# Kernel optimization log

Hardware: AMD Instinct MI355X
Metric: run time of the kernel (lower is better)

The kernel has to match this reference:

```python
import jax, jax.numpy as jnp
import numpy as np
from jax.scipy.special import erf

T_OBS = 1.0
T_CONTROL = 3.0
B = 4096
NT = 2048
DT0 = 0.002


def _moments(t_obs):
    t_avg = t_obs / 2.0
    t2_avg = t_obs ** 2 / 3.0
    C_t = t2_avg - t_avg ** 2
    return t_avg, t2_avg, C_t


def _sigma_move(sig_f, sig_a, xi_f, xi_v, t_obs):
    # 3x3 posterior covariance over (a, f, v), per get_Sigma_move_noSM
    xi_f_ = xi_f * (np.sqrt(t_obs) / sig_f)
    xi_v_ = xi_v * (np.sqrt(t_obs) / sig_f)
    t_avg, t2_avg, C_t = _moments(t_obs)
    det_inv = (1 + 1 / xi_f_ ** 2) * (C_t + 1 / xi_v_ ** 2) + t_avg ** 2 / xi_f_ ** 2
    pre = sig_f ** 2 / t_obs / det_inv ** 2
    Sff = (C_t + 1 / xi_v_ ** 2) ** 2 + C_t * t_avg ** 2
    Sfv = t_avg * (1 / (xi_f_ * xi_v_) ** 2 - C_t)
    Svv = (t_avg / xi_f_ ** 2) ** 2 + C_t * (1 + 1 / xi_f_ ** 2) ** 2
    zz = jnp.zeros(())
    row0 = jnp.stack([sig_a ** 2, zz, zz])
    row1 = jnp.stack([zz, pre * Sff, pre * Sfv])
    row2 = jnp.stack([zz, pre * Sfv, pre * Svv])
    return jnp.stack([row0, row1, row2])


def _sigma_stat(sig_f, xi_f, xi_v, t_obs):
    # 2x2 posterior covariance over (f, v), per get_Sigma_stat_noSM
    xi_f_ = xi_f * (np.sqrt(t_obs) / sig_f)
    xi_v_ = xi_v * (np.sqrt(t_obs) / sig_f)
    t_avg, t2_avg, C_t = _moments(t_obs)
    det_inv = (1 + 1 / xi_f_ ** 2) * (C_t + 1 / xi_v_ ** 2) + t_avg ** 2 / xi_f_ ** 2
    pre = sig_f ** 2 / t_obs
    Sff = pre / (1 + 1 / xi_f_ ** 2) ** 2
    Sfv = pre * (t_avg / (xi_f_ ** 2 + 1)) / det_inv
    Svv = pre * ((t_avg / xi_f_ ** 2) ** 2 + C_t * (1 + 1 / xi_f_ ** 2) ** 2) / det_inv ** 2
    return jnp.stack([jnp.stack([Sff, Sfv]), jnp.stack([Sfv, Svv])])


def _threshold(sig_f, xi_f, xi_v, d0, t_obs):
    xi_f_ = xi_f * (np.sqrt(t_obs) / sig_f)
    xi_v_ = xi_v * (np.sqrt(t_obs) / sig_f)
    t_avg, t2_avg, C_t = _moments(t_obs)
    log_arg = 1 + xi_v_ ** 2 * (C_t + t2_avg / (1 + xi_f_ ** 2))
    det_ratio = t_obs / sig_f ** 2 * (C_t + 1 / xi_v_ ** 2 + t2_avg / (1 + xi_f_ ** 2))
    thresh_sq = (jnp.log(log_arg) - 2 * d0) / det_ratio
    return jnp.sqrt(jax.nn.relu(thresh_sq))


def _control_weights(tau, t_wait, alpha, T_control):
    # Control-A gain profiles over the (shared) time grid tau [NT].
    Tm = T_control - jnp.mean(t_wait)
    rem = jax.nn.relu(Tm - tau)
    w_f = alpha * rem / Tm
    w_v = alpha * rem ** 2 / (2 * Tm ** 2)
    w_o_move = jnp.stack([w_f, w_v])          # [2, NT]
    w_o_stat = w_f[None, :]                   # [1, NT]
    w_tx = alpha * jnp.ones_like(tau)         # [NT]
    w_tv = alpha * rem / Tm                   # [NT]
    return w_o_move, w_o_stat, w_tx, w_tv


def _get_L(u_t, x_t, z, dt, Sinv_m, Sinv_s, det_m, det_s, W_m, W_s, q,
           wo_m, wo_s, w_tx, w_tv, g, sig_a):
    z_noa = z[:, 1:]
    num_t = u_t.shape[1]
    g2 = g * g
    resid = u_t - w_tx[None, :] * x_t                          # [B, T]
    data_quad = 0.5 * (dt / g2) * jnp.sum(resid ** 2, axis=-1)  # [B]

    def branch(Sinv, W, zz, wo, with_ctrl_v):
        S_vv = Sinv[-1, -1]
        S_vo = Sinv[-1, :-1]
        S_oo = Sinv[:-1, :-1]
        W_v = W[-1]
        W_o = W[:-1]
        A = S_oo[None] + (dt[:, None, None] / g2) * (wo @ wo.T)[None]  # [B,no,no]
        A_inv = jnp.linalg.inv(A)
        det_A = jnp.linalg.det(A)
        Woz = zz @ W_o.T                                       # [B, no]
        Wvz = zz @ W_v                                         # [B]
        d = (dt[:, None] / g2) * jnp.einsum('it,bt->bi', wo, resid)
        J_r = Woz @ S_oo.T + Wvz[:, None] * S_vo[None, :] + d   # [B, no]
        if with_ctrl_v:
            J_v = S_vo[None, :] + (dt[:, None] / g2) * (wo @ w_tv)[None, :]
            J = (S_vv * Wvz + Woz @ S_vo
                 + (dt / g2) * jnp.einsum('t,bt->b', w_tv, resid)
                 - jnp.einsum('bi,bij,bj->b', J_r, A_inv, J_v))
            k = (S_vv + (dt / g2) * jnp.sum(w_tv ** 2)
                 - jnp.einsum('bi,bij,bj->b', J_v, A_inv, J_v))
        else:
            J_v = jnp.broadcast_to(S_vo[None, :], J_r.shape)
            J = (S_vv * Wvz + Woz @ S_vo
                 - jnp.einsum('bi,bij,bj->b', J_r, A_inv, J_v))
            k = S_vv - jnp.einsum('bi,bij,bj->b', J_v, A_inv, J_v)
        Z = (0.5 * jnp.einsum('bi,ij,jk,kl,bl->b', zz, W, Sinv, W, zz)
             + data_quad
             - 0.5 * jnp.einsum('bi,bij,bj->b', J_r, A_inv, J_r)
             - 0.5 * J * J / k)
        return J, k, Z, det_A

    J_m, k_m, Z_m, detA_m = branch(Sinv_m, W_m, z, wo_m, True)
    J_s, k_s, Z_s, detA_s = branch(Sinv_s, W_s, z_noa, wo_s, False)

    pre_m = k_m * detA_m * det_m * sig_a ** 2
    pre_s = k_s * detA_s * det_s
    erf_m = (1 + 0.5 * erf((J_m - k_m * q) / jnp.sqrt(2 * k_m))
             - 0.5 * erf((J_m + k_m * q) / jnp.sqrt(2 * k_m)))
    erf_s = (0.5 * erf((J_s + k_s * q) / jnp.sqrt(2 * k_s))
             - 0.5 * erf((J_s - k_s * q) / jnp.sqrt(2 * k_s)))
    L_m = jnp.exp(-Z_m) * erf_m / jnp.sqrt(pre_m)
    L_s = jnp.exp(-Z_s) * erf_s / jnp.sqrt(pre_s)
    return jnp.sum(num_t * jnp.log(2 * np.pi * g2 / dt) - jnp.log(L_m + L_s))


def _forward(u_t, x_t, z, t, t_wait, u_t_SM, x_t_SM, z_SM, t_SM, t_wait_SM,
             hsig_f, hsig_w, hxi_f, hxi_w, hxi_v, delta0, halpha, hg, hW_aa, hsig_a):
    sig_f = jnp.exp(hsig_f[0]); sig_w = jnp.exp(hsig_w[0])
    xi_f = jnp.exp(hxi_f[0]); xi_w = jnp.exp(hxi_w[0]); xi_v = jnp.exp(hxi_v[0])
    d0 = delta0[0]; alpha = jnp.exp(halpha[0]); g = jnp.exp(hg[0])
    W_aa = jnp.exp(hW_aa[0]); sig_a = jnp.exp(hsig_a[0])
    one = jnp.ones(())

    dt = t[:, 1] - t[:, 0]
    dt_SM = t_SM[:, 1] - t[:, 0]  # matches original code (uses t[:,0])

    # ---- no self-motion branch ----
    Sig_m = _sigma_move(sig_f, sig_a, xi_f, xi_v, T_OBS)
    Sig_s = _sigma_stat(sig_f, xi_f, xi_v, T_OBS)
    Sinv_m = jnp.linalg.inv(Sig_m); det_m = jnp.linalg.det(Sig_m)
    Sinv_s = jnp.linalg.inv(Sig_s); det_s = jnp.linalg.det(Sig_s)
    W_m = jnp.diag(jnp.stack([W_aa, one, alpha]))
    W_s = jnp.diag(jnp.stack([one, alpha]))
    q = _threshold(sig_f, xi_f, xi_v, d0, T_OBS)
    wo_m, wo_s, w_tx, w_tv = _control_weights(t[0], t_wait, alpha, T_CONTROL)
    L1 = _get_L(u_t, x_t, z, dt, Sinv_m, Sinv_s, det_m, det_s,
                W_m, W_s, q, wo_m, wo_s, w_tx, w_tv, g, sig_a)

    # ---- self-motion branch: noise inflated by sig_w / xi_w, gain scaled by W_aa ----
    sig_eff = jnp.sqrt(sig_f ** 2 + sig_w ** 2)
    xi_v_eff = jnp.sqrt(xi_v ** 2 + xi_w ** 2)
    alpha_sm = alpha * W_aa
    Sig_m2 = _sigma_move(sig_eff, sig_a, xi_f, xi_v_eff, T_OBS)
    Sig_s2 = _sigma_stat(sig_eff, xi_f, xi_v_eff, T_OBS)
    Sinv_m2 = jnp.linalg.inv(Sig_m2); det_m2 = jnp.linalg.det(Sig_m2)
    Sinv_s2 = jnp.linalg.inv(Sig_s2); det_s2 = jnp.linalg.det(Sig_s2)
    W_m2 = jnp.diag(jnp.stack([W_aa, one, alpha_sm]))
    W_s2 = jnp.diag(jnp.stack([one, alpha_sm]))
    q2 = _threshold(sig_eff, xi_f, xi_v_eff, d0, T_OBS)
    wo_m2, wo_s2, w_tx2, w_tv2 = _control_weights(t_SM[0], t_wait_SM, alpha_sm, T_CONTROL)
    L2 = _get_L(u_t_SM, x_t_SM, z_SM, dt_SM, Sinv_m2, Sinv_s2, det_m2, det_s2,
                W_m2, W_s2, q2, wo_m2, wo_s2, w_tx2, w_tv2, g, sig_a)
    return L1 + L2


def setup_inputs() -> dict:
    key = jax.random.key(0)
    ks = jax.random.split(key, 8)
    f32 = jnp.float32
    tau = jnp.arange(NT, dtype=f32) * DT0
    t = jnp.broadcast_to(tau, (B, NT))
    return {
        'u_t': 0.05 * jax.random.normal(ks[0], (B, NT), f32),
        'x_t': 0.05 * jax.random.normal(ks[1], (B, NT), f32),
        'z': 0.1 * jax.random.normal(ks[2], (B, 3), f32),
        't': t,
        't_wait': 0.3 * jax.random.uniform(ks[3], (B,), f32),
        'u_t_SM': 0.05 * jax.random.normal(ks[4], (B, NT), f32),
        'x_t_SM': 0.05 * jax.random.normal(ks[5], (B, NT), f32),
        'z_SM': 0.1 * jax.random.normal(ks[6], (B, 3), f32),
        't_SM': t,
        't_wait_SM': 0.3 * jax.random.uniform(ks[7], (B,), f32),
        'hsig_f': jnp.array([-0.7], f32),
        'hsig_w': jnp.array([-1.0], f32),
        'hxi_f': jnp.array([0.0], f32),
        'hxi_w': jnp.array([-0.5], f32),
        'hxi_v': jnp.array([0.0], f32),
        'delta0': jnp.array([-0.5], f32),
        'halpha': jnp.array([-0.3], f32),
        'hg': jnp.array([0.0], f32),
        'hW_aa': jnp.array([-0.2], f32),
        'hsig_a': jnp.array([-0.7], f32),
    }


def reference(u_t, x_t, z, t, t_wait, u_t_SM, x_t_SM, z_SM, t_SM, t_wait_SM,
              hsig_f, hsig_w, hxi_f, hxi_w, hxi_v, delta0, halpha, hg, hW_aa, hsig_a):
    return _forward(u_t, x_t, z, t, t_wait, u_t_SM, x_t_SM, z_SM, t_SM, t_wait_SM,
                    hsig_f, hsig_w, hxi_f, hxi_w, hxi_v, delta0, halpha, hg, hW_aa, hsig_a)
```

## Files before the change

kernel.cpp:

```cpp
#include <hip/hip_runtime.h>
#include <math.h>

#ifndef M_PI
#define M_PI 3.14159265358979323846
#endif

#define TPB 256


__device__ double block_sum_d(double v, double* buf) {
    int tid = threadIdx.x;
    buf[tid] = v;
    __syncthreads();
    for (int o = TPB / 2; o > 0; o >>= 1) {
        if (tid < o) buf[tid] += buf[tid + o];
        __syncthreads();
    }
    double r = buf[0];
    __syncthreads();
    return r;
}

__global__ __launch_bounds__(TPB) void precompute_kernel(
    const float* __restrict__ t, const float* __restrict__ t_wait,
    const float* __restrict__ t_SM, const float* __restrict__ t_wait_SM,
    const float* __restrict__ hsig_f, const float* __restrict__ hsig_w,
    const float* __restrict__ hxi_f, const float* __restrict__ hxi_w,
    const float* __restrict__ hxi_v, const float* __restrict__ delta0,
    const float* __restrict__ halpha, const float* __restrict__ hg,
    const float* __restrict__ hW_aa, const float* __restrict__ hsig_a,
    int B, int NT, double* __restrict__ ws, float* __restrict__ out)
{
    __shared__ double buf[TPB];
    __shared__ double sh[2];
    int tid = threadIdx.x;

    double s1 = 0.0, s2 = 0.0;
    for (int i = tid; i < B; i += TPB) {
        s1 += (double)t_wait[i];
        s2 += (double)t_wait_SM[i];
    }
    double tw1 = block_sum_d(s1, buf);
    double tw2 = block_sum_d(s2, buf);
    if (tid == 0) { sh[0] = 3.0 - tw1 / (double)B; sh[1] = 3.0 - tw2 / (double)B; }
    __syncthreads();
    double Tm1 = sh[0], Tm2 = sh[1];

    double a2 = 0, a3 = 0, a4 = 0, b2 = 0, b3 = 0, b4 = 0;
    for (int i = tid; i < NT; i += TPB) {
        double r1 = Tm1 - (double)t[i];    r1 = r1 > 0.0 ? r1 : 0.0;
        double r2 = Tm2 - (double)t_SM[i]; r2 = r2 > 0.0 ? r2 : 0.0;
        double r1s = r1 * r1, r2s = r2 * r2;
        a2 += r1s; a3 += r1s * r1; a4 += r1s * r1s;
        b2 += r2s; b3 += r2s * r2; b4 += r2s * r2s;
    }
    a2 = block_sum_d(a2, buf); a3 = block_sum_d(a3, buf); a4 = block_sum_d(a4, buf);
    b2 = block_sum_d(b2, buf); b3 = block_sum_d(b3, buf); b4 = block_sum_d(b4, buf);
    if (tid != 0) return;

    out[0] = 0.0f;

    double sig_f = exp((double)hsig_f[0]);
    double sig_w = exp((double)hsig_w[0]);
    double xi_f  = exp((double)hxi_f[0]);
    double xi_w  = exp((double)hxi_w[0]);
    double xi_v  = exp((double)hxi_v[0]);
    double d0    = (double)delta0[0];
    double alpha = exp((double)halpha[0]);
    double g     = exp((double)hg[0]);
    double W_aa  = exp((double)hW_aa[0]);
    double sig_a = exp((double)hsig_a[0]);
    double g2 = g * g, sig_a2 = sig_a * sig_a;

    for (int L = 0; L < 2; ++L) {
        double sf, xv, ab, Tm, S2, S3, S4;
        if (L == 0) { sf = sig_f; xv = xi_v; ab = alpha; Tm = Tm1; S2 = a2; S3 = a3; S4 = a4; }
        else {
            sf = sqrt(sig_f * sig_f + sig_w * sig_w);
            xv = sqrt(xi_v * xi_v + xi_w * xi_w);
            ab = alpha * W_aa; Tm = Tm2; S2 = b2; S3 = b3; S4 = b4;
        }
        double xf_ = xi_f / sf, xv_ = xv / sf;
        double t_avg = 0.5, t2_avg = 1.0 / 3.0, C_t = 1.0 / 12.0;
        double ixf2 = 1.0 / (xf_ * xf_), ixv2 = 1.0 / (xv_ * xv_);
        double det_inv = (1.0 + ixf2) * (C_t + ixv2) + t_avg * t_avg * ixf2;

        double pre_m = sf * sf / (det_inv * det_inv);
        double Sff = (C_t + ixv2) * (C_t + ixv2) + C_t * t_avg * t_avg;
        double Sfv = t_avg * (ixf2 * ixv2 - C_t);
        double Svv = (t_avg * ixf2) * (t_avg * ixf2) + C_t * (1.0 + ixf2) * (1.0 + ixf2);
        double m11 = pre_m * Sff, m12 = pre_m * Sfv, m22 = pre_m * Svv;
        double detB = m11 * m22 - m12 * m12;
        double Sm00 = 1.0 / sig_a2;
        double Sm11 = m22 / detB, Sm12 = -m12 / detB, Sm22 = m11 / detB;
        double det_m = sig_a2 * detB;

        double pre_s = sf * sf;
        double Sffs = pre_s / ((1.0 + ixf2) * (1.0 + ixf2));
        double Sfvs = pre_s * (t_avg / (xf_ * xf_ + 1.0)) / det_inv;
        double Svvs = pre_s * ((t_avg * ixf2) * (t_avg * ixf2) + C_t * (1.0 + ixf2) * (1.0 + ixf2)) / (det_inv * det_inv);
        double det_s = Sffs * Svvs - Sfvs * Sfvs;
        double Ss00 = Svvs / det_s, Ss01 = -Sfvs / det_s, Ss11 = Sffs / det_s;

        double log_arg = 1.0 + xv_ * xv_ * (C_t + t2_avg / (1.0 + xf_ * xf_));
        double det_ratio = (1.0 / (sf * sf)) * (C_t + 1.0 / (xv_ * xv_) + t2_avg / (1.0 + xf_ * xf_));
        double tq = (log(log_arg) - 2.0 * d0) / det_ratio;
        double q = sqrt(tq > 0.0 ? tq : 0.0);

        double kf = ab / Tm, kv = ab / (2.0 * Tm * Tm);
        double Gff = kf * kf * S2, Gfv = kf * kv * S3, Gvv = kv * kv * S4;

        double* w = ws + L * 32;
        w[0] = Sm00; w[1] = 0.0; w[2] = 0.0; w[3] = Sm11; w[4] = Sm12; w[5] = Sm22;
        w[6] = Ss00; w[7] = Ss01; w[8] = Ss11;
        w[9] = det_m; w[10] = det_s; w[11] = q;
        w[12] = Gff; w[13] = Gfv; w[14] = Gvv;
        w[15] = ab; w[16] = kf; w[17] = kv; w[18] = Tm;
        w[19] = W_aa; w[20] = g2; w[21] = sig_a2;
    }
}

__global__ __launch_bounds__(TPB) void stream_kernel(
    const float* __restrict__ u_t, const float* __restrict__ x_t,
    const float* __restrict__ u_SM, const float* __restrict__ x_SM,
    const float* __restrict__ t, const float* __restrict__ t_SM,
    int NT, int B, const double* __restrict__ ws, float* __restrict__ mom)
{
    int wid  = blockIdx.x * (TPB / 64) + (threadIdx.x >> 6);
    int lane = threadIdx.x & 63;
    int row  = wid >> 1, half = wid & 1;
    int n4 = NT >> 2, h4 = n4 >> 1;

    float ab1 = (float)ws[15],      Tm1 = (float)ws[18];
    float ab2 = (float)ws[32 + 15], Tm2 = (float)ws[32 + 18];

    size_t off = (size_t)row * (size_t)NT;
    const float4* U1 = (const float4*)(u_t + off);
    const float4* X1 = (const float4*)(x_t + off);
    const float4* U2 = (const float4*)(u_SM + off);
    const float4* X2 = (const float4*)(x_SM + off);
    const float4* T1 = (const float4*)t;
    const float4* T2 = (const float4*)t_SM;

    float s2a = 0, r1a = 0, r2a = 0, s2b = 0, r1b = 0, r2b = 0;
    int iend = (half + 1) * h4;
    for (int i = half * h4 + lane; i < iend; i += 64) {
        float4 u = U1[i], x = X1[i], ta = T1[i];
        float4 uu = U2[i], xx = X2[i], tb = T2[i];
        float uc[4]  = {u.x, u.y, u.z, u.w};
        float xc[4]  = {x.x, x.y, x.z, x.w};
        float tc[4]  = {ta.x, ta.y, ta.z, ta.w};
        float uuc[4] = {uu.x, uu.y, uu.z, uu.w};
        float xxc[4] = {xx.x, xx.y, xx.z, xx.w};
        float tbc[4] = {tb.x, tb.y, tb.z, tb.w};
#pragma unroll
        for (int j = 0; j < 4; ++j) {
            float resid = fmaf(-ab1, xc[j], uc[j]);
            float rem = fmaxf(Tm1 - tc[j], 0.0f);
            s2a = fmaf(resid, resid, s2a);
            r1a = fmaf(rem, resid, r1a);
            r2a = fmaf(rem * rem, resid, r2a);
            float rs = fmaf(-ab2, xxc[j], uuc[j]);
            float rm = fmaxf(Tm2 - tbc[j], 0.0f);
            s2b = fmaf(rs, rs, s2b);
            r1b = fmaf(rm, rs, r1b);
            r2b = fmaf(rm * rm, rs, r2b);
        }
    }
#pragma unroll
    for (int o = 32; o >= 1; o >>= 1) {
        s2a += __shfl_xor(s2a, o); r1a += __shfl_xor(r1a, o); r2a += __shfl_xor(r2a, o);
        s2b += __shfl_xor(s2b, o); r1b += __shfl_xor(r1b, o); r2b += __shfl_xor(r2b, o);
    }
    if (lane == 0) {
        int W = 2 * B;
        mom[0 * W + wid] = s2a; mom[1 * W + wid] = r1a; mom[2 * W + wid] = r2a;
        mom[3 * W + wid] = s2b; mom[4 * W + wid] = r1b; mom[5 * W + wid] = r2b;
    }
}

__device__ double epilogue(const double* __restrict__ S, int NT,
                           double s2, double R1, double R2,
                           double z0, double z1, double z2, double dtb)
{
    double Sm00 = S[0], Sm01 = S[1], Sm02 = S[2], Sm11 = S[3], Sm12 = S[4], Sm22 = S[5];
    double Ss00 = S[6], Ss01 = S[7], Ss11 = S[8];
    double det_m = S[9], det_s = S[10], q = S[11];
    double Gff = S[12], Gfv = S[13], Gvv = S[14];
    double ab = S[15], kf = S[16], kv = S[17];
    double W_aa = S[19], g2 = S[20], sig_a2 = S[21];

    double cb = dtb / g2;
    double df = kf * R1, dv = kv * R2;
    double data_quad = 0.5 * cb * s2;

    double Svo0 = Sm02, Svo1 = Sm12, Svv = Sm22;
    double A00 = Sm00 + cb * Gff, A01 = Sm01 + cb * Gfv, A11 = Sm11 + cb * Gvv;
    double detA = A00 * A11 - A01 * A01;
    double i00 = A11 / detA, i01 = -A01 / detA, i11 = A00 / detA;
    double Woz0 = W_aa * z0, Woz1 = z1, Wvz = ab * z2;
    double Jr0 = Woz0 * Sm00 + Woz1 * Sm01 + Wvz * Svo0 + cb * df;
    double Jr1 = Woz0 * Sm01 + Woz1 * Sm11 + Wvz * Svo1 + cb * dv;
    double Jv0 = Svo0 + cb * Gff, Jv1 = Svo1 + cb * Gfv;
    double AiJv0 = i00 * Jv0 + i01 * Jv1, AiJv1 = i01 * Jv0 + i11 * Jv1;
    double AiJr0 = i00 * Jr0 + i01 * Jr1, AiJr1 = i01 * Jr0 + i11 * Jr1;
    double Jm = Svv * Wvz + Woz0 * Svo0 + Woz1 * Svo1 + cb * df
              - (Jr0 * AiJv0 + Jr1 * AiJv1);
    double km = Svv + cb * Gff - (Jv0 * AiJv0 + Jv1 * AiJv1);
    double y0 = W_aa * z0, y1 = z1, y2 = ab * z2;
    double zq = y0 * y0 * Sm00 + y1 * y1 * Sm11 + y2 * y2 * Sm22
              + 2.0 * (y0 * y1 * Sm01 + y0 * y2 * Sm02 + y1 * y2 * Sm12);
    double Zm = 0.5 * zq + data_quad - 0.5 * (Jr0 * AiJr0 + Jr1 * AiJr1) - 0.5 * Jm * Jm / km;

    double As = Ss00 + cb * Gff;
    double Wozs = z1, Wvzs = ab * z2;
    double Jrs = Wozs * Ss00 + Wvzs * Ss01 + cb * df;
    double Jvs = Ss01;
    double Js = Ss11 * Wvzs + Wozs * Ss01 - Jrs * Jvs / As;
    double ks = Ss11 - Jvs * Jvs / As;
    double ys1 = ab * z2;
    double zqs = z1 * z1 * Ss00 + 2.0 * z1 * ys1 * Ss01 + ys1 * ys1 * Ss11;
    double Zs = 0.5 * zqs + data_quad - 0.5 * Jrs * Jrs / As - 0.5 * Js * Js / ks;

    double pre_m = km * detA * det_m * sig_a2;
    double pre_s = ks * As * det_s;
    double sm = sqrt(2.0 * km), ss = sqrt(2.0 * ks);
    double em = 1.0 + 0.5 * erf((Jm - km * q) / sm) - 0.5 * erf((Jm + km * q) / sm);
    double es = 0.5 * erf((Js + ks * q) / ss) - 0.5 * erf((Js - ks * q) / ss);
    double Lm = exp(-Zm) * em / sqrt(pre_m);
    double Ls = exp(-Zs) * es / sqrt(pre_s);
    return (double)NT * log(2.0 * M_PI * g2 / dtb) - log(Lm + Ls);
}

__global__ __launch_bounds__(TPB) void epilogue_kernel(
    const float* __restrict__ z, const float* __restrict__ z_SM,
    const float* __restrict__ t, const float* __restrict__ t_SM,
    int NT, int B, const double* __restrict__ ws,
    const float* __restrict__ mom, float* __restrict__ out)
{
    int row = blockIdx.x * TPB + threadIdx.x;
    double c = 0.0;
    if (row < B) {
        int W = 2 * B;
        double S2a = (double)mom[0 * W + 2 * row] + (double)mom[0 * W + 2 * row + 1];
        double R1a = (double)mom[1 * W + 2 * row] + (double)mom[1 * W + 2 * row + 1];
        double R2a = (double)mom[2 * W + 2 * row] + (double)mom[2 * W + 2 * row + 1];
        double S2b = (double)mom[3 * W + 2 * row] + (double)mom[3 * W + 2 * row + 1];
        double R1b = (double)mom[4 * W + 2 * row] + (double)mom[4 * W + 2 * row + 1];
        double R2b = (double)mom[5 * W + 2 * row] + (double)mom[5 * W + 2 * row + 1];
        size_t off = (size_t)row * (size_t)NT;
        double dtb1 = (double)t[off + 1] - (double)t[off];
        double dtb2 = (double)t_SM[off + 1] - (double)t[off];
        double z0 = (double)z[row * 3 + 0], z1 = (double)z[row * 3 + 1], z2 = (double)z[row * 3 + 2];
        double w0 = (double)z_SM[row * 3 + 0], w1 = (double)z_SM[row * 3 + 1], w2 = (double)z_SM[row * 3 + 2];
        c = epilogue(ws, NT, S2a, R1a, R2a, z0, z1, z2, dtb1)
          + epilogue(ws + 32, NT, S2b, R1b, R2b, w0, w1, w2, dtb2);
    }
    __shared__ double buf[TPB];
    int tid = threadIdx.x;
    buf[tid] = c;
    __syncthreads();
    for (int o = TPB / 2; o > 0; o >>= 1) {
        if (tid < o) buf[tid] += buf[tid + o];
        __syncthreads();
    }
    if (tid == 0) atomicAdd(out, (float)buf[0]);
}

extern "C" void kernel_launch(void* const* d_in, const int* in_sizes, int n_in,
                              void* d_out, int out_size, void* d_ws, size_t ws_size,
                              hipStream_t stream) {
    const float* u_t       = (const float*)d_in[0];
    const float* x_t       = (const float*)d_in[1];
    const float* z         = (const float*)d_in[2];
    const float* t         = (const float*)d_in[3];
    const float* t_wait    = (const float*)d_in[4];
    const float* u_t_SM    = (const float*)d_in[5];
    const float* x_t_SM    = (const float*)d_in[6];
    const float* z_SM      = (const float*)d_in[7];
    const float* t_SM      = (const float*)d_in[8];
    const float* t_wait_SM = (const float*)d_in[9];
    const float* hsig_f = (const float*)d_in[10];
    const float* hsig_w = (const float*)d_in[11];
    const float* hxi_f  = (const float*)d_in[12];
    const float* hxi_w  = (const float*)d_in[13];
    const float* hxi_v  = (const float*)d_in[14];
    const float* delta0 = (const float*)d_in[15];
    const float* halpha = (const float*)d_in[16];
    const float* hg     = (const float*)d_in[17];
    const float* hW_aa  = (const float*)d_in[18];
    const float* hsig_a = (const float*)d_in[19];

    int B  = in_sizes[4];
    int NT = in_sizes[0] / B;

    double* ws  = (double*)d_ws;
    float*  mom = (float*)(ws + 64);
    float*  out = (float*)d_out;

    precompute_kernel<<<1, TPB, 0, stream>>>(t, t_wait, t_SM, t_wait_SM,
        hsig_f, hsig_w, hxi_f, hxi_w, hxi_v, delta0, halpha, hg, hW_aa, hsig_a,
        B, NT, ws, out);

    int nwaves = 2 * B;
    int nblocks = nwaves / (TPB / 64);
    stream_kernel<<<nblocks, TPB, 0, stream>>>(u_t, x_t, u_t_SM, x_t_SM, t, t_SM,
        NT, B, ws, mom);

    epilogue_kernel<<<(B + TPB - 1) / TPB, TPB, 0, stream>>>(z, z_SM, t, t_SM,
        NT, B, ws, mom, out);
}
```

Baseline: 240.9 us.

## Assign one block per row and unroll streaming loads two-deep

The streaming kernel now gives each row a whole 256-thread block instead of two 64-lane half-row waves. Each thread issues two sets of float4 loads per iteration to raise memory-level parallelism, and wave partials are combined through shared memory into a row-major per-row moment buffer. The epilogue reads six contiguous moments per row. With NT=2048 each thread covers only two float4s, so the added LDS reduction and __syncthreads per row may offset the gain from more outstanding loads.

```diff
diff --git a/kernel.cpp b/kernel.cpp
--- a/kernel.cpp
+++ b/kernel.cpp
@@ -124,58 +124,94 @@
     const float* __restrict__ u_t, const float* __restrict__ x_t,
     const float* __restrict__ u_SM, const float* __restrict__ x_SM,
     const float* __restrict__ t, const float* __restrict__ t_SM,
-    int NT, int B, const double* __restrict__ ws, float* __restrict__ mom)
+    int NT, const double* __restrict__ ws, float* __restrict__ mom)
 {
-    int wid  = blockIdx.x * (TPB / 64) + (threadIdx.x >> 6);
-    int lane = threadIdx.x & 63;
-    int row  = wid >> 1, half = wid & 1;
-    int n4 = NT >> 2, h4 = n4 >> 1;
-
+    int b = blockIdx.x, tid = threadIdx.x;
     float ab1 = (float)ws[15],      Tm1 = (float)ws[18];
     float ab2 = (float)ws[32 + 15], Tm2 = (float)ws[32 + 18];
 
-    size_t off = (size_t)row * (size_t)NT;
+    size_t off = (size_t)b * (size_t)NT;
     const float4* U1 = (const float4*)(u_t + off);
     const float4* X1 = (const float4*)(x_t + off);
     const float4* U2 = (const float4*)(u_SM + off);
     const float4* X2 = (const float4*)(x_SM + off);
     const float4* T1 = (const float4*)t;
     const float4* T2 = (const float4*)t_SM;
+    int n4 = NT >> 2;
 
     float s2a = 0, r1a = 0, r2a = 0, s2b = 0, r1b = 0, r2b = 0;
-    int iend = (half + 1) * h4;
-    for (int i = half * h4 + lane; i < iend; i += 64) {
-        float4 u = U1[i], x = X1[i], ta = T1[i];
-        float4 uu = U2[i], xx = X2[i], tb = T2[i];
-        float uc[4]  = {u.x, u.y, u.z, u.w};
-        float xc[4]  = {x.x, x.y, x.z, x.w};
-        float tc[4]  = {ta.x, ta.y, ta.z, ta.w};
-        float uuc[4] = {uu.x, uu.y, uu.z, uu.w};
-        float xxc[4] = {xx.x, xx.y, xx.z, xx.w};
-        float tbc[4] = {tb.x, tb.y, tb.z, tb.w};
+
+    for (int i = tid; i < n4; i += 2 * TPB) {
+        int j = i + TPB;
+        bool hasj = j < n4;
+        float4 uA = U1[i], xA = X1[i], tA = T1[i];
+        float4 vA = U2[i], yA = X2[i], sA = T2[i];
+        float4 uB, xB, tB, vB, yB, sB;
+        if (hasj) {
+            uB = U1[j]; xB = X1[j]; tB = T1[j];
+            vB = U2[j]; yB = X2[j]; sB = T2[j];
+        }
+        {
+            float uc[4]  = {uA.x, uA.y, uA.z, uA.w};
+            float xc[4]  = {xA.x, xA.y, xA.z, xA.w};
+            float tc[4]  = {tA.x, tA.y, tA.z, tA.w};
+            float uuc[4] = {vA.x, vA.y, vA.z, vA.w};
+            float xxc[4] = {yA.x, yA.y, yA.z, yA.w};
+            float tbc[4] = {sA.x, sA.y, sA.z, sA.w};
 #pragma unroll
-        for (int j = 0; j < 4; ++j) {
-            float resid = fmaf(-ab1, xc[j], uc[j]);
-            float rem = fmaxf(Tm1 - tc[j], 0.0f);
-            s2a = fmaf(resid, resid, s2a);
-            r1a = fmaf(rem, resid, r1a);
-            r2a = fmaf(rem * rem, resid, r2a);
-            float rs = fmaf(-ab2, xxc[j], uuc[j]);
-            float rm = fmaxf(Tm2 - tbc[j], 0.0f);
-            s2b = fmaf(rs, rs, s2b);
-            r1b = fmaf(rm, rs, r1b);
-            r2b = fmaf(rm * rm, rs, r2b);
+            for (int k = 0; k < 4; ++k) {
+                float resid = fmaf(-ab1, xc[k], uc[k]);
+                float rem = fmaxf(Tm1 - tc[k], 0.0f);
+                s2a = fmaf(resid, resid, s2a);
+                r1a = fmaf(rem, resid, r1a);
+                r2a = fmaf(rem * rem, resid, r2a);
+                float rs = fmaf(-ab2, xxc[k], uuc[k]);
+                float rm = fmaxf(Tm2 - tbc[k], 0.0f);
+                s2b = fmaf(rs, rs, s2b);
+                r1b = fmaf(rm, rs, r1b);
+                r2b = fmaf(rm * rm, rs, r2b);
+            }
         }
-    }
+        if (hasj) {
+            float uc[4]  = {uB.x, uB.y, uB.z, uB.w};
+            float xc[4]  = {xB.x, xB.y, xB.z, xB.w};
+            float tc[4]  = {tB.x, tB.y, tB.z, tB.w};
+            float uuc[4] = {vB.x, vB.y, vB.z, vB.w};
+            float xxc[4] = {yB.x, yB.y, yB.z, yB.w};
+            float tbc[4] = {sB.x, sB.y, sB.z, sB.w};
+#pragma unroll
+            for (int k = 0; k < 4; ++k) {
+                float resid = fmaf(-ab1, xc[k], uc[k]);
+                float rem = fmaxf(Tm1 - tc[k], 0.0f);
+                s2a = fmaf(resid, resid, s2a);
+                r1a = fmaf(rem, resid, r1a);
+                r2a = fmaf(rem * rem, resid, r2a);
+                float rs = fmaf(-ab2, xxc[k], uuc[k]);
+                float rm = fmaxf(Tm2 - tbc[k], 0.0f);
+                s2b = fmaf(rs, rs, s2b);
+                r1b = fmaf(rm, rs, r1b);
+                r2b = fmaf(rm * rm, rs, r2b);
+            }
+        }
+    }
+
 #pragma unroll
     for (int o = 32; o >= 1; o >>= 1) {
         s2a += __shfl_xor(s2a, o); r1a += __shfl_xor(r1a, o); r2a += __shfl_xor(r2a, o);
         s2b += __shfl_xor(s2b, o); r1b += __shfl_xor(r1b, o); r2b += __shfl_xor(r2b, o);
     }
+    __shared__ float red[TPB / 64][6];
+    int wave = tid >> 6, lane = tid & 63;
     if (lane == 0) {
-        int W = 2 * B;
-        mom[0 * W + wid] = s2a; mom[1 * W + wid] = r1a; mom[2 * W + wid] = r2a;
-        mom[3 * W + wid] = s2b; mom[4 * W + wid] = r1b; mom[5 * W + wid] = r2b;
+        red[wave][0] = s2a; red[wave][1] = r1a; red[wave][2] = r2a;
+        red[wave][3] = s2b; red[wave][4] = r1b; red[wave][5] = r2b;
+    }
+    __syncthreads();
+    if (tid < 6) {
+        float acc = 0.0f;
+#pragma unroll
+        for (int w = 0; w < TPB / 64; ++w) acc += red[w][tid];
+        mom[b * 6 + tid] = acc;
     }
 }
 
@@ -241,13 +277,12 @@
     int row = blockIdx.x * TPB + threadIdx.x;
     double c = 0.0;
     if (row < B) {
-        int W = 2 * B;
-        double S2a = (double)mom[0 * W + 2 * row] + (double)mom[0 * W + 2 * row + 1];
-        double R1a = (double)mom[1 * W + 2 * row] + (double)mom[1 * W + 2 * row + 1];
-        double R2a = (double)mom[2 * W + 2 * row] + (double)mom[2 * W + 2 * row + 1];
-        double S2b = (double)mom[3 * W + 2 * row] + (double)mom[3 * W + 2 * row + 1];
-        double R1b = (double)mom[4 * W + 2 * row] + (double)mom[4 * W + 2 * row + 1];
-        double R2b = (double)mom[5 * W + 2 * row] + (double)mom[5 * W + 2 * row + 1];
+        double S2a = (double)mom[row * 6 + 0];
+        double R1a = (double)mom[row * 6 + 1];
+        double R2a = (double)mom[row * 6 + 2];
+        double S2b = (double)mom[row * 6 + 3];
+        double R1b = (double)mom[row * 6 + 4];
+        double R2b = (double)mom[row * 6 + 5];
         size_t off = (size_t)row * (size_t)NT;
         double dtb1 = (double)t[off + 1] - (double)t[off];
         double dtb2 = (double)t_SM[off + 1] - (double)t[off];
@@ -302,10 +337,8 @@
         hsig_f, hsig_w, hxi_f, hxi_w, hxi_v, delta0, halpha, hg, hW_aa, hsig_a,
         B, NT, ws, out);
 
-    int nwaves = 2 * B;
-    int nblocks = nwaves / (TPB / 64);
-    stream_kernel<<<nblocks, TPB, 0, stream>>>(u_t, x_t, u_t_SM, x_t_SM, t, t_SM,
-        NT, B, ws, mom);
+    stream_kernel<<<B, TPB, 0, stream>>>(u_t, x_t, u_t_SM, x_t_SM, t, t_SM,
+        NT, ws, mom);
 
     epilogue_kernel<<<(B + TPB - 1) / TPB, TPB, 0, stream>>>(z, z_SM, t, t_SM,
         NT, B, ws, mom, out);
```

After: 241.1 us. Within noise of the previous version (+0.1%).

## Flatten streaming pass into grid-stride loop with per-wave atomic row accumulation

Applied to the files above, without the earlier changes.

Replaces the per-row, two-waves-per-row streaming kernel with a flat grid-stride kernel capped at 2048 blocks. It processes the two datasets in separate passes, reduces each wave with shuffles and atomically adds the partial moments into a per-row buffer that the precompute kernel now zeroes. The aim is better load balance and fewer resident waves with a persistent-style grid. In exchange it issues three float atomics per wave per iteration, loses the fused dual-stream loop, and makes the summation order nondeterministic.

```diff
diff --git a/kernel.cpp b/kernel.cpp
--- a/kernel.cpp
+++ b/kernel.cpp
@@ -29,11 +29,14 @@
     const float* __restrict__ hxi_v, const float* __restrict__ delta0,
     const float* __restrict__ halpha, const float* __restrict__ hg,
     const float* __restrict__ hW_aa, const float* __restrict__ hsig_a,
-    int B, int NT, double* __restrict__ ws, float* __restrict__ out)
+    int B, int NT, double* __restrict__ ws, float* __restrict__ mom,
+    float* __restrict__ out)
 {
     __shared__ double buf[TPB];
     __shared__ double sh[2];
     int tid = threadIdx.x;
+
+    for (int i = tid; i < B * 6; i += TPB) mom[i] = 0.0f;
 
     double s1 = 0.0, s2 = 0.0;
     for (int i = tid; i < B; i += TPB) {
@@ -120,63 +123,64 @@
     }
 }
 
-__global__ __launch_bounds__(TPB) void stream_kernel(
+__device__ __forceinline__ void flat_pass(
+    const float4* __restrict__ U, const float4* __restrict__ X,
+    const float4* __restrict__ T, float ab, float Tm,
+    long total4, long gtid, long nthr, int lane, int rshift, int cmask,
+    float* __restrict__ mom, int mom_off)
+{
+    for (long f = gtid; f < total4; f += nthr) {
+        float4 u = U[f];
+        float4 x = X[f];
+        int col = (int)(f & cmask);
+        float4 tt = T[col];
+        float uc[4] = {u.x, u.y, u.z, u.w};
+        float xc[4] = {x.x, x.y, x.z, x.w};
+        float tc[4] = {tt.x, tt.y, tt.z, tt.w};
+        float s2 = 0.0f, r1 = 0.0f, r2 = 0.0f;
+#pragma unroll
+        for (int k = 0; k < 4; ++k) {
+            float resid = fmaf(-ab, xc[k], uc[k]);
+            float rem = fmaxf(Tm - tc[k], 0.0f);
+            s2 = fmaf(resid, resid, s2);
+            r1 = fmaf(rem, resid, r1);
+            r2 = fmaf(rem * rem, resid, r2);
+        }
+#pragma unroll
+        for (int o = 32; o >= 1; o >>= 1) {
+            s2 += __shfl_xor(s2, o);
+            r1 += __shfl_xor(r1, o);
+            r2 += __shfl_xor(r2, o);
+        }
+        if (lane == 0) {
+            int row = (int)(f >> rshift);
+            float* m = mom + (size_t)row * 6 + mom_off;
+            atomicAdd(m + 0, s2);
+            atomicAdd(m + 1, r1);
+            atomicAdd(m + 2, r2);
+        }
+    }
+}
+
+__global__ __launch_bounds__(TPB) void flat_kernel(
     const float* __restrict__ u_t, const float* __restrict__ x_t,
     const float* __restrict__ u_SM, const float* __restrict__ x_SM,
     const float* __restrict__ t, const float* __restrict__ t_SM,
-    int NT, int B, const double* __restrict__ ws, float* __restrict__ mom)
-{
-    int wid  = blockIdx.x * (TPB / 64) + (threadIdx.x >> 6);
+    int rshift, long total4, const double* __restrict__ ws,
+    float* __restrict__ mom)
+{
+    long gtid = (long)blockIdx.x * TPB + threadIdx.x;
+    long nthr = (long)gridDim.x * TPB;
     int lane = threadIdx.x & 63;
-    int row  = wid >> 1, half = wid & 1;
-    int n4 = NT >> 2, h4 = n4 >> 1;
+    int cmask = (1 << rshift) - 1;
 
     float ab1 = (float)ws[15],      Tm1 = (float)ws[18];
     float ab2 = (float)ws[32 + 15], Tm2 = (float)ws[32 + 18];
 
-    size_t off = (size_t)row * (size_t)NT;
-    const float4* U1 = (const float4*)(u_t + off);
-    const float4* X1 = (const float4*)(x_t + off);
-    const float4* U2 = (const float4*)(u_SM + off);
-    const float4* X2 = (const float4*)(x_SM + off);
-    const float4* T1 = (const float4*)t;
-    const float4* T2 = (const float4*)t_SM;
-
-    float s2a = 0, r1a = 0, r2a = 0, s2b = 0, r1b = 0, r2b = 0;
-    int iend = (half + 1) * h4;
-    for (int i = half * h4 + lane; i < iend; i += 64) {
-        float4 u = U1[i], x = X1[i], ta = T1[i];
-        float4 uu = U2[i], xx = X2[i], tb = T2[i];
-        float uc[4]  = {u.x, u.y, u.z, u.w};
-        float xc[4]  = {x.x, x.y, x.z, x.w};
-        float tc[4]  = {ta.x, ta.y, ta.z, ta.w};
-        float uuc[4] = {uu.x, uu.y, uu.z, uu.w};
-        float xxc[4] = {xx.x, xx.y, xx.z, xx.w};
-        float tbc[4] = {tb.x, tb.y, tb.z, tb.w};
-#pragma unroll
-        for (int j = 0; j < 4; ++j) {
-            float resid = fmaf(-ab1, xc[j], uc[j]);
-            float rem = fmaxf(Tm1 - tc[j], 0.0f);
-            s2a = fmaf(resid, resid, s2a);
-            r1a = fmaf(rem, resid, r1a);
-            r2a = fmaf(rem * rem, resid, r2a);
-            float rs = fmaf(-ab2, xxc[j], uuc[j]);
-            float rm = fmaxf(Tm2 - tbc[j], 0.0f);
-            s2b = fmaf(rs, rs, s2b);
-            r1b = fmaf(rm, rs, r1b);
-            r2b = fmaf(rm * rm, rs, r2b);
-        }
-    }
-#pragma unroll
-    for (int o = 32; o >= 1; o >>= 1) {
-        s2a += __shfl_xor(s2a, o); r1a += __shfl_xor(r1a, o); r2a += __shfl_xor(r2a, o);
-        s2b += __shfl_xor(s2b, o); r1b += __shfl_xor(r1b, o); r2b += __shfl_xor(r2b, o);
-    }
-    if (lane == 0) {
-        int W = 2 * B;
-        mom[0 * W + wid] = s2a; mom[1 * W + wid] = r1a; mom[2 * W + wid] = r2a;
-        mom[3 * W + wid] = s2b; mom[4 * W + wid] = r1b; mom[5 * W + wid] = r2b;
-    }
+    flat_pass((const float4*)u_t,  (const float4*)x_t,  (const float4*)t,
+              ab1, Tm1, total4, gtid, nthr, lane, rshift, cmask, mom, 0);
+    flat_pass((const float4*)u_SM, (const float4*)x_SM, (const float4*)t_SM,
+              ab2, Tm2, total4, gtid, nthr, lane, rshift, cmask, mom, 3);
 }
 
 __device__ double epilogue(const double* __restrict__ S, int NT,
@@ -241,13 +245,12 @@
     int row = blockIdx.x * TPB + threadIdx.x;
     double c = 0.0;
     if (row < B) {
-        int W = 2 * B;
-        double S2a = (double)mom[0 * W + 2 * row] + (double)mom[0 * W + 2 * row + 1];
-        double R1a = (double)mom[1 * W + 2 * row] + (double)mom[1 * W + 2 * row + 1];
-        double R2a = (double)mom[2 * W + 2 * row] + (double)mom[2 * W + 2 * row + 1];
-        double S2b = (double)mom[3 * W + 2 * row] + (double)mom[3 * W + 2 * row + 1];
-        double R1b = (double)mom[4 * W + 2 * row] + (double)mom[4 * W + 2 * row + 1];
-        double R2b = (double)mom[5 * W + 2 * row] + (double)mom[5 * W + 2 * row + 1];
+        double S2a = (double)mom[row * 6 + 0];
+        double R1a = (double)mom[row * 6 + 1];
+        double R2a = (double)mom[row * 6 + 2];
+        double S2b = (double)mom[row * 6 + 3];
+        double R1b = (double)mom[row * 6 + 4];
+        double R2b = (double)mom[row * 6 + 5];
         size_t off = (size_t)row * (size_t)NT;
         double dtb1 = (double)t[off + 1] - (double)t[off];
         double dtb2 = (double)t_SM[off + 1] - (double)t[off];
@@ -300,12 +303,16 @@
 
     precompute_kernel<<<1, TPB, 0, stream>>>(t, t_wait, t_SM, t_wait_SM,
         hsig_f, hsig_w, hxi_f, hxi_w, hxi_v, delta0, halpha, hg, hW_aa, hsig_a,
-        B, NT, ws, out);
-
-    int nwaves = 2 * B;
-    int nblocks = nwaves / (TPB / 64);
-    stream_kernel<<<nblocks, TPB, 0, stream>>>(u_t, x_t, u_t_SM, x_t_SM, t, t_SM,
-        NT, B, ws, mom);
+        B, NT, ws, mom, out);
+
+    int n4 = NT >> 2;
+    int rshift = 0;
+    while ((1 << rshift) < n4) ++rshift;
+    long total4 = (long)B * (long)n4;
+    long want_blocks = (total4 + TPB - 1) / TPB;
+    int nblocks = (int)(want_blocks < 2048 ? want_blocks : 2048);
+    flat_kernel<<<nblocks, TPB, 0, stream>>>(u_t, x_t, u_t_SM, x_t_SM, t, t_SM,
+        rshift, total4, ws, mom);
 
     epilogue_kernel<<<(B + TPB - 1) / TPB, TPB, 0, stream>>>(z, z_SM, t, t_SM,
         NT, B, ws, mom, out);
```

Result: slower. 247.6 us (+2.8%).
